# Performance work log

Hardware: AMD Instinct MI355X
Metric: run time of the kernel (lower is better)

Reference implementation:

```python
import jax, jax.numpy as jnp
import numpy as np
from jax import lax

B, S, H, T = 64, 512, 1024, 67


def setup_inputs() -> dict:
    key = jax.random.key(0)
    ks = jax.random.split(key, 8)
    hidden = jax.random.normal(ks[0], (B, S, H), jnp.float32)
    labels = jax.random.randint(ks[1], (B, S), 0, T)
    lengths = jax.random.randint(ks[2], (B,), S // 2, S + 1)
    mask = (jnp.arange(S)[None, :] < lengths[:, None]).astype(jnp.int32)  # prefix mask, mask[:,0]=1
    W = jax.random.normal(ks[3], (H, T), jnp.float32) * 0.02
    b = jnp.zeros((T,), jnp.float32)
    start_trans = jax.random.uniform(ks[4], (T,), jnp.float32, -0.1, 0.1)
    end_trans = jax.random.uniform(ks[5], (T,), jnp.float32, -0.1, 0.1)
    trans = jax.random.uniform(ks[6], (T, T), jnp.float32, -0.1, 0.1)
    return dict(hidden=hidden, labels=labels, mask=mask, W=W, b=b,
                start_trans=start_trans, end_trans=end_trans, trans=trans)


def _crf_llh(em, tags, mask, start_trans, end_trans, trans):
    # em: (B,S,T), tags: (B,S) int, mask: (B,S) bool. torchcrf log-likelihood per sequence.
    maskf = mask.astype(em.dtype)
    # numerator: score of the gold path
    em_tag = jnp.take_along_axis(em, tags[:, :, None], axis=2)[:, :, 0]       # (B,S)
    num = start_trans[tags[:, 0]] + em_tag[:, 0]
    trans_tag = trans[tags[:, :-1], tags[:, 1:]]                              # (B,S-1)
    num = num + jnp.sum((trans_tag + em_tag[:, 1:]) * maskf[:, 1:], axis=1)
    last_idx = jnp.sum(mask.astype(jnp.int32), axis=1) - 1                    # (B,)
    last_tags = jnp.take_along_axis(tags, last_idx[:, None], axis=1)[:, 0]
    num = num + end_trans[last_tags]
    # denominator: log partition via forward algorithm (scan over time)
    def step(score, x):
        em_i, m_i = x  # (B,T), (B,)
        nxt = jax.nn.logsumexp(score[:, :, None] + trans[None] + em_i[:, None, :], axis=1)
        return jnp.where(m_i[:, None], nxt, score), None
    init = start_trans[None, :] + em[:, 0]
    score, _ = lax.scan(step, init, (em[:, 1:].transpose(1, 0, 2), mask[:, 1:].T))
    denom = jax.nn.logsumexp(score + end_trans[None, :], axis=1)
    return num - denom


def _viterbi(em, mask, start_trans, end_trans, trans):
    # returns best tag sequence (B,S), padded positions set to 0
    n_tags = em.shape[-1]
    ident = jnp.arange(n_tags)[None, :]
    def fwd(score, x):
        em_i, m_i = x  # (B,T), (B,)
        cand = score[:, :, None] + trans[None]                                # (B,T,T)
        idx = jnp.argmax(cand, axis=1)                                        # (B,T)
        nxt = jnp.max(cand, axis=1) + em_i
        score = jnp.where(m_i[:, None], nxt, score)
        idx = jnp.where(m_i[:, None], idx, ident)  # identity link on padded steps
        return score, idx
    init = start_trans[None, :] + em[:, 0]
    score, hist = lax.scan(fwd, init, (em[:, 1:].transpose(1, 0, 2), mask[:, 1:].T))
    best = jnp.argmax(score + end_trans[None, :], axis=1)                     # (B,)
    def back(carry, h):  # carry = tag at t+1, h = hist[t]: (B,T)
        prev = jnp.take_along_axis(h, carry[:, None], axis=1)[:, 0]
        return prev, prev
    _, ys = lax.scan(back, best, hist, reverse=True)                          # (S-1,B) tags[0..S-2]
    tags = jnp.concatenate([ys.transpose(1, 0), best[:, None]], axis=1)       # (B,S)
    return jnp.where(mask, tags, 0)


def reference(hidden, labels, mask, W, b, start_trans, end_trans, trans):
    maskb = mask.astype(bool)
    # dropout is identity in eval mode
    em = jnp.einsum('bsh,ht->bst', jax.nn.leaky_relu(hidden, 0.01), W) + b     # token_scores
    llh = _crf_llh(em, labels, maskb, start_trans, end_trans, trans)
    loss = -jnp.sum(llh) / em.shape[0]
    tags = _viterbi(em, maskb, start_trans, end_trans, trans)
    return loss, tags, em
```

## Files before the change

kernel.cpp:

```cpp
#include <hip/hip_runtime.h>

#define Bn 64
#define Sn 512
#define Hn 1024
#define Tn 67

#define LOG2E 1.4426950408889634f
#define LN2   0.6931471805599453f

__global__ __launch_bounds__(256) void gemm_em(
    const float* __restrict__ hidden, const float* __restrict__ W,
    const float* __restrict__ bias, float* __restrict__ em,
    float* __restrict__ out)
{
    __shared__ __align__(16) float hs[64][36];
    __shared__ __align__(16) float wt[80][36];

    const int tid = threadIdx.x;
    const int tx = tid & 15, ty = tid >> 4;
    const int row0 = blockIdx.x * 64;

    if (blockIdx.x == 0 && tid == 0) out[0] = 0.0f;

    float acc[4][5];
#pragma unroll
    for (int u = 0; u < 4; ++u)
#pragma unroll
        for (int v = 0; v < 5; ++v) acc[u][v] = 0.f;

    for (int kc = 0; kc < Hn; kc += 32) {
#pragma unroll
        for (int l = 0; l < 2; ++l) {
            int idx = tid + l * 256;
            int r = idx >> 3, kq = (idx & 7) << 2;
            float4 v = *reinterpret_cast<const float4*>(
                &hidden[(size_t)(row0 + r) * Hn + kc + kq]);
            v.x = v.x > 0.f ? v.x : 0.01f * v.x;
            v.y = v.y > 0.f ? v.y : 0.01f * v.y;
            v.z = v.z > 0.f ? v.z : 0.01f * v.z;
            v.w = v.w > 0.f ? v.w : 0.01f * v.w;
            *reinterpret_cast<float4*>(&hs[r][kq]) = v;
        }
        for (int idx = tid; idx < 32 * Tn; idx += 256) {
            int k = idx / Tn;
            int t = idx - k * Tn;
            wt[t][k] = W[(size_t)(kc + k) * Tn + t];
        }
        __syncthreads();

#pragma unroll
        for (int k0 = 0; k0 < 32; k0 += 4) {
            float4 hv[4], wv[5];
#pragma unroll
            for (int u = 0; u < 4; ++u)
                hv[u] = *reinterpret_cast<float4*>(&hs[ty + 16 * u][k0]);
#pragma unroll
            for (int v = 0; v < 5; ++v)
                wv[v] = *reinterpret_cast<float4*>(&wt[tx + 16 * v][k0]);
#pragma unroll
            for (int u = 0; u < 4; ++u)
#pragma unroll
                for (int v = 0; v < 5; ++v) {
                    acc[u][v] = fmaf(hv[u].x, wv[v].x, acc[u][v]);
                    acc[u][v] = fmaf(hv[u].y, wv[v].y, acc[u][v]);
                    acc[u][v] = fmaf(hv[u].z, wv[v].z, acc[u][v]);
                    acc[u][v] = fmaf(hv[u].w, wv[v].w, acc[u][v]);
                }
        }
        __syncthreads();
    }

#pragma unroll
    for (int v = 0; v < 5; ++v) {
        int c = tx + 16 * v;
        if (c < Tn) {
            float bb = bias[c];
#pragma unroll
            for (int u = 0; u < 4; ++u) {
                int row = row0 + ty + 16 * u;
                em[(size_t)row * Tn + c] = acc[u][v] + bb;
            }
        }
    }
}

__device__ __forceinline__ unsigned long long shflx64(unsigned long long v, int m) {
    unsigned int lo = (unsigned int)v, hi = (unsigned int)(v >> 32);
    lo = __shfl_xor(lo, m);
    hi = __shfl_xor(hi, m);
    return ((unsigned long long)hi << 32) | lo;
}

__device__ __forceinline__ unsigned long long packkey(float v, int idx) {
    unsigned int b = __float_as_uint(v);
    unsigned int s = b ^ (unsigned int)(((int)b >> 31) | 0x80000000);
    return ((unsigned long long)s << 32) | (unsigned int)(127 - idx);
}

__device__ __forceinline__ float unpackval(unsigned long long key) {
    unsigned int s = (unsigned int)(key >> 32);
    unsigned int b = s ^ (unsigned int)((~(int)s >> 31) | 0x80000000);
    return __uint_as_float(b);
}

__global__ __launch_bounds__(192, 1) void crf_scan5(
    const float* __restrict__ em, const int* __restrict__ labels,
    const int* __restrict__ mask, const float* __restrict__ startT,
    const float* __restrict__ endT, const float* __restrict__ trans,
    float* __restrict__ out)
{
    __shared__ __align__(16) float emC[2][1088];
    __shared__ __align__(16) float emV[2][1088];
    __shared__ int maskC[Sn];
    __shared__ int maskV[Sn];
    __shared__ __align__(16) float pb[2][72];
    __shared__ __align__(16) float vb[2][72];
    __shared__ unsigned char hist[Sn - 1][68];
    __shared__ int tg[Sn];
    __shared__ float numSh;
    __shared__ int lenSh;

    const int tid = threadIdx.x;
    const int wid = tid >> 6;
    const int lane = tid & 63;
    const int b = blockIdx.x;
    const float* emg = em + (size_t)b * Sn * Tn;
    const int u2 = lane < 3 ? lane : 2;
    const int st2 = 64 + u2;

    if (wid == 0) {
#pragma unroll
        for (int i = 0; i < 8; ++i)
            maskC[lane + i * 64] = mask[b * Sn + lane + i * 64];

        float Ec1[68], Ec2[68];
#pragma unroll
        for (int i = 0; i < Tn; ++i) {
            Ec1[i] = exp2f(trans[i * Tn + lane] * LOG2E);
            Ec2[i] = exp2f(trans[i * Tn + st2] * LOG2E);
        }
        Ec1[67] = 0.f; Ec2[67] = 0.f;

        float sreg[17];
#pragma unroll
        for (int i = 0; i < 17; ++i) { int idx = lane + i * 64; if (idx > 1071) idx = 1071; sreg[i] = emg[idx]; }
#pragma unroll
        for (int i = 0; i < 17; ++i) {
            int idx = lane + i * 64;
            if (idx < 1072) { int s = idx / 67; emC[0][s * 68 + (idx - s * 67)] = sreg[i]; }
        }
#pragma unroll
        for (int i = 0; i < 17; ++i) { int idx = lane + i * 64; if (idx > 1071) idx = 1071; sreg[i] = emg[1072 + idx]; }

        if (lane == 0) { pb[0][67] = 0.f; pb[1][67] = 0.f; }

        float sc1 = startT[lane] + emC[0][lane];
        float sc2 = startT[st2] + emC[0][st2];
        float M = __shfl(sc1, 0);
        float p1 = exp2f((sc1 - M) * LOG2E);
        float p2 = exp2f((sc2 - M) * LOG2E);
        pb[0][lane] = p1;
        if (lane < 3) pb[0][64 + lane] = p2;
        float Mprev = M;

        for (int t = 1; t < Sn; ++t) {
            const int cb = (t >> 4) & 1;
            if ((t & 15) == 0) {
                const int k = t >> 4;
#pragma unroll
                for (int i = 0; i < 17; ++i) {
                    int idx = lane + i * 64;
                    if (idx < 1072) { int s = idx / 67; emC[cb][s * 68 + (idx - s * 67)] = sreg[i]; }
                }
                if (k < 31) {
                    const float* src = emg + (size_t)(k + 1) * 1072;
#pragma unroll
                    for (int i = 0; i < 17; ++i) { int idx = lane + i * 64; if (idx > 1071) idx = 1071; sreg[i] = src[idx]; }
                }
            }
            const float* row = &emC[cb][(t & 15) * 68];
            float em1 = row[lane];
            float em2 = row[st2];
            int m = maskC[t];
            const float4* P = (const float4*)&pb[(t + 1) & 1][0];
            float a0 = 0, a1 = 0, a2 = 0, a3 = 0, c0 = 0, c1 = 0, c2 = 0, c3 = 0;
#pragma unroll
            for (int q = 0; q < 17; ++q) {
                float4 pv = P[q];
                a0 = fmaf(pv.x, Ec1[4 * q + 0], a0); c0 = fmaf(pv.x, Ec2[4 * q + 0], c0);
                a1 = fmaf(pv.y, Ec1[4 * q + 1], a1); c1 = fmaf(pv.y, Ec2[4 * q + 1], c1);
                a2 = fmaf(pv.z, Ec1[4 * q + 2], a2); c2 = fmaf(pv.z, Ec2[4 * q + 2], c2);
                a3 = fmaf(pv.w, Ec1[4 * q + 3], a3); c3 = fmaf(pv.w, Ec2[4 * q + 3], c3);
            }
            float s1 = (a0 + a1) + (a2 + a3);
            float s2 = (c0 + c1) + (c2 + c3);
            float n1 = Mprev + log2f(s1) * LN2 + em1;
            float n2 = Mprev + log2f(s2) * LN2 + em2;
            if (m) { sc1 = n1; sc2 = n2; }
            M = __shfl(sc1, 0);
            p1 = exp2f((sc1 - M) * LOG2E);
            p2 = exp2f((sc2 - M) * LOG2E);
            float* Wp = &pb[t & 1][0];
            Wp[lane] = p1;
            if (lane < 3) Wp[64 + lane] = p2;
            Mprev = M;
        }

        float* F = &pb[0][0];
        F[lane] = sc1 + endT[lane];
        if (lane < 3) F[64 + lane] = sc2 + endT[64 + lane];
        if (lane == 0) F[67] = -1e30f;
        float mx = -1e30f;
        const float4* Fv = (const float4*)F;
#pragma unroll
        for (int q = 0; q < 17; ++q) {
            float4 v = Fv[q];
            mx = fmaxf(mx, fmaxf(fmaxf(v.x, v.y), fmaxf(v.z, v.w)));
        }
        float ss = 0.f;
#pragma unroll
        for (int q = 0; q < 17; ++q) {
            float4 v = Fv[q];
            ss += exp2f((v.x - mx) * LOG2E) + exp2f((v.y - mx) * LOG2E)
                + exp2f((v.z - mx) * LOG2E) + exp2f((v.w - mx) * LOG2E);
        }
        float denom = mx + log2f(ss) * LN2;
        __syncthreads();
        if (lane == 0) {
            int len = lenSh;
            float num = numSh + endT[labels[b * Sn + len - 1]];
            atomicAdd(out, -(num - denom) * (1.0f / (float)Bn));
        }
    } else if (wid == 1) {
#pragma unroll
        for (int i = 0; i < 8; ++i)
            maskV[lane + i * 64] = mask[b * Sn + lane + i * 64];

        float Tc1[68];
#pragma unroll
        for (int i = 0; i < Tn; ++i) Tc1[i] = trans[i * Tn + lane];
        Tc1[67] = 0.f;
        float Tsf[3], Tss[3];
        const int rsec = (lane < 3) ? (64 + lane) : 0;
#pragma unroll
        for (int u = 0; u < 3; ++u) {
            Tsf[u] = trans[lane * Tn + 64 + u];
            Tss[u] = trans[rsec * Tn + 64 + u];
        }

        float sreg[17];
#pragma unroll
        for (int i = 0; i < 17; ++i) { int idx = lane + i * 64; if (idx > 1071) idx = 1071; sreg[i] = emg[idx]; }
#pragma unroll
        for (int i = 0; i < 17; ++i) {
            int idx = lane + i * 64;
            if (idx < 1072) { int s = idx / 67; emV[0][s * 68 + (idx - s * 67)] = sreg[i]; }
        }
#pragma unroll
        for (int i = 0; i < 17; ++i) { int idx = lane + i * 64; if (idx > 1071) idx = 1071; sreg[i] = emg[1072 + idx]; }

        float sc1 = startT[lane] + emV[0][lane];
        float sc2 = startT[st2] + emV[0][st2];
        vb[0][lane] = sc1;
        if (lane < 3) vb[0][64 + lane] = sc2;
        if (lane == 0) { vb[0][67] = -1e30f; vb[1][67] = -1e30f; }

        for (int t = 1; t < Sn; ++t) {
            const int cb = (t >> 4) & 1;
            if ((t & 15) == 0) {
                const int k = t >> 4;
#pragma unroll
                for (int i = 0; i < 17; ++i) {
                    int idx = lane + i * 64;
                    if (idx < 1072) { int s = idx / 67; emV[cb][s * 68 + (idx - s * 67)] = sreg[i]; }
                }
                if (k < 31) {
                    const float* src = emg + (size_t)(k + 1) * 1072;
#pragma unroll
                    for (int i = 0; i < 17; ++i) { int idx = lane + i * 64; if (idx > 1071) idx = 1071; sreg[i] = src[idx]; }
                }
            }
            const float* row = &emV[cb][(t & 15) * 68];
            float em1 = row[lane];
            float e64 = row[64], e65 = row[65], e66 = row[66];
            int m = maskV[t];

            const float4* Vp = (const float4*)&vb[(t + 1) & 1][0];
            float bvv[34]; int bx[34];
#pragma unroll
            for (int q = 0; q < 17; ++q) {
                float4 v = Vp[q];
                float c0 = v.x + Tc1[4 * q + 0];
                float c1 = v.y + Tc1[4 * q + 1];
                float c2 = v.z + Tc1[4 * q + 2];
                float c3 = v.w + Tc1[4 * q + 3];
                bool r0 = c1 > c0;
                bvv[2 * q]     = r0 ? c1 : c0;
                bx[2 * q]      = r0 ? 4 * q + 1 : 4 * q + 0;
                bool r1 = c3 > c2;
                bvv[2 * q + 1] = r1 ? c3 : c2;
                bx[2 * q + 1]  = r1 ? 4 * q + 3 : 4 * q + 2;
            }
#pragma unroll
            for (int q = 0; q < 17; ++q) {
                bool r = bvv[2 * q + 1] > bvv[2 * q];
                bvv[q] = r ? bvv[2 * q + 1] : bvv[2 * q];
                bx[q]  = r ? bx[2 * q + 1]  : bx[2 * q];
            }
#pragma unroll
            for (int q = 0; q < 8; ++q) {
                bool r = bvv[2 * q + 1] > bvv[2 * q];
                bvv[q] = r ? bvv[2 * q + 1] : bvv[2 * q];
                bx[q]  = r ? bx[2 * q + 1]  : bx[2 * q];
            }
            bvv[8] = bvv[16]; bx[8] = bx[16];
#pragma unroll
            for (int q = 0; q < 4; ++q) {
                bool r = bvv[2 * q + 1] > bvv[2 * q];
                bvv[q] = r ? bvv[2 * q + 1] : bvv[2 * q];
                bx[q]  = r ? bx[2 * q + 1]  : bx[2 * q];
            }
            bvv[4] = bvv[8]; bx[4] = bx[8];
#pragma unroll
            for (int q = 0; q < 2; ++q) {
                bool r = bvv[2 * q + 1] > bvv[2 * q];
                bvv[q] = r ? bvv[2 * q + 1] : bvv[2 * q];
                bx[q]  = r ? bx[2 * q + 1]  : bx[2 * q];
            }
            bvv[2] = bvv[4]; bx[2] = bx[4];
            { bool r = bvv[1] > bvv[0]; bvv[0] = r ? bvv[1] : bvv[0]; bx[0] = r ? bx[1] : bx[0]; }
            { bool r = bvv[2] > bvv[0]; bvv[0] = r ? bvv[2] : bvv[0]; bx[0] = r ? bx[2] : bx[0]; }
            float n1 = bvv[0] + em1;

            float ca = sc1 + Tsf[0]; int ia = lane;
            float cbv = sc1 + Tsf[1]; int ib = lane;
            float cc = sc1 + Tsf[2]; int ic = lane;
            if (lane < 3) {
                float sa = sc2 + Tss[0]; if (sa > ca)  { ca = sa;  ia = 64 + lane; }
                float sb = sc2 + Tss[1]; if (sb > cbv) { cbv = sb; ib = 64 + lane; }
                float scv = sc2 + Tss[2]; if (scv > cc) { cc = scv; ic = 64 + lane; }
            }
            unsigned long long k0 = packkey(ca, ia);
            unsigned long long k1 = packkey(cbv, ib);
            unsigned long long k2 = packkey(cc, ic);
#pragma unroll
            for (int k = 1; k < 64; k <<= 1) {
                unsigned long long o0 = shflx64(k0, k); if (o0 > k0) k0 = o0;
                unsigned long long o1 = shflx64(k1, k); if (o1 > k1) k1 = o1;
                unsigned long long o2 = shflx64(k2, k); if (o2 > k2) k2 = o2;
            }
            float v64 = unpackval(k0) + e64;
            float v65 = unpackval(k1) + e65;
            float v66 = unpackval(k2) + e66;
            int i64 = 127 - (int)(unsigned int)(k0 & 0xffffffffu);
            int i65 = 127 - (int)(unsigned int)(k1 & 0xffffffffu);
            int i66 = 127 - (int)(unsigned int)(k2 & 0xffffffffu);

            float nuv = (lane == 0) ? v64 : (lane == 1) ? v65 : v66;
            int nui = (lane == 0) ? i64 : (lane == 1) ? i65 : i66;

            int idx1 = m ? bx[0] : lane;
            int idx2 = m ? nui : st2;
            if (m) { sc1 = n1; sc2 = nuv; }

            hist[t - 1][lane] = (unsigned char)idx1;
            float* Wv = &vb[t & 1][0];
            Wv[lane] = sc1;
            if (lane < 3) {
                hist[t - 1][64 + lane] = (unsigned char)idx2;
                Wv[64 + lane] = sc2;
            }
        }

        float* F = &vb[0][0];
        F[lane] = sc1 + endT[lane];
        if (lane < 3) F[64 + lane] = sc2 + endT[64 + lane];
        if (lane == 0) F[67] = -1e30f;
        const float4* Fv = (const float4*)F;
        float bvv[34]; int bx[34];
#pragma unroll
        for (int q = 0; q < 17; ++q) {
            float4 v = Fv[q];
            bool r0 = v.y > v.x;
            bvv[2 * q]     = r0 ? v.y : v.x;
            bx[2 * q]      = r0 ? 4 * q + 1 : 4 * q + 0;
            bool r1 = v.w > v.z;
            bvv[2 * q + 1] = r1 ? v.w : v.z;
            bx[2 * q + 1]  = r1 ? 4 * q + 3 : 4 * q + 2;
        }
#pragma unroll
        for (int q = 0; q < 17; ++q) {
            bool r = bvv[2 * q + 1] > bvv[2 * q];
            bvv[q] = r ? bvv[2 * q + 1] : bvv[2 * q];
            bx[q]  = r ? bx[2 * q + 1]  : bx[2 * q];
        }
#pragma unroll
        for (int q = 0; q < 8; ++q) {
            bool r = bvv[2 * q + 1] > bvv[2 * q];
            bvv[q] = r ? bvv[2 * q + 1] : bvv[2 * q];
            bx[q]  = r ? bx[2 * q + 1]  : bx[2 * q];
        }
        bvv[8] = bvv[16]; bx[8] = bx[16];
#pragma unroll
        for (int q = 0; q < 4; ++q) {
            bool r = bvv[2 * q + 1] > bvv[2 * q];
            bvv[q] = r ? bvv[2 * q + 1] : bvv[2 * q];
            bx[q]  = r ? bx[2 * q + 1]  : bx[2 * q];
        }
        bvv[4] = bvv[8]; bx[4] = bx[8];
#pragma unroll
        for (int q = 0; q < 2; ++q) {
            bool r = bvv[2 * q + 1] > bvv[2 * q];
            bvv[q] = r ? bvv[2 * q + 1] : bvv[2 * q];
            bx[q]  = r ? bx[2 * q + 1]  : bx[2 * q];
        }
        bvv[2] = bvv[4]; bx[2] = bx[4];
        { bool r = bvv[1] > bvv[0]; bvv[0] = r ? bvv[1] : bvv[0]; bx[0] = r ? bx[1] : bx[0]; }
        { bool r = bvv[2] > bvv[0]; bvv[0] = r ? bvv[2] : bvv[0]; bx[0] = r ? bx[2] : bx[0]; }

        if (lane == 0) {
            int carry = bx[0];
            tg[Sn - 1] = carry;
            for (int k = Sn - 2; k >= 0; --k) {
                carry = hist[k][carry];
                tg[k] = carry;
            }
        }
        float* tagsOut = out + 1 + b * Sn;
#pragma unroll
        for (int i = 0; i < 8; ++i) {
            int s = lane + i * 64;
            tagsOut[s] = maskV[s] ? (float)tg[s] : 0.f;
        }
        __syncthreads();
    } else {
        float part = 0.f; int lenp = 0;
#pragma unroll
        for (int i = 0; i < 8; ++i) {
            int s = lane + i * 64;
            int ms = mask[b * Sn + s];
            lenp += ms;
            int ls = labels[b * Sn + s];
            if (s == 0) {
                part += startT[ls] + emg[ls];
            } else if (ms) {
                int lp = labels[b * Sn + s - 1];
                part += trans[lp * Tn + ls] + emg[(size_t)s * Tn + ls];
            }
        }
#pragma unroll
        for (int k = 1; k < 64; k <<= 1) {
            part += __shfl_xor(part, k);
            lenp += __shfl_xor(lenp, k);
        }
        if (lane == 0) { numSh = part; lenSh = lenp; }
        __syncthreads();
    }
}

extern "C" void kernel_launch(void* const* d_in, const int* in_sizes, int n_in,
                              void* d_out, int out_size, void* d_ws, size_t ws_size,
                              hipStream_t stream) {
    const float* hidden = (const float*)d_in[0];
    const int*   labels = (const int*)d_in[1];
    const int*   maskp  = (const int*)d_in[2];
    const float* W      = (const float*)d_in[3];
    const float* bias   = (const float*)d_in[4];
    const float* startT = (const float*)d_in[5];
    const float* endT   = (const float*)d_in[6];
    const float* trans  = (const float*)d_in[7];
    float* out = (float*)d_out;
    float* em  = out + 1 + (size_t)Bn * Sn;

    hipLaunchKernelGGL(gemm_em, dim3((Bn * Sn) / 64), dim3(256), 0, stream,
                       hidden, W, bias, em, out);
    hipLaunchKernelGGL(crf_scan5, dim3(Bn), dim3(192), 0, stream,
                       em, labels, maskp, startT, endT, trans, out);
}
```

Baseline: 789.3 us.

## Move transition matrices from registers to LDS and reduce tail columns via shuffles

The exp-transition and raw-transition columns that each lane held in registers now live in float4-packed LDS tables read per step. The three tail tags (64-66) in the forward pass are no longer a second 68-wide dot product per lane. Each lane computes three partial products and a wavefront butterfly reduction sums them. The Viterbi argmax tree also fuses its first two levels to shorten the per-step chain. This trims register pressure and redundant FMAs, but adds LDS reads and a six-stage shuffle chain to every serial scan step.

```diff
diff --git a/kernel.cpp b/kernel.cpp
--- a/kernel.cpp
+++ b/kernel.cpp
@@ -103,7 +103,7 @@
     return __uint_as_float(b);
 }
 
-__global__ __launch_bounds__(192, 1) void crf_scan5(
+__global__ __launch_bounds__(192, 1) void crf_scan6(
     const float* __restrict__ em, const int* __restrict__ labels,
     const int* __restrict__ mask, const float* __restrict__ startT,
     const float* __restrict__ endT, const float* __restrict__ trans,
@@ -115,6 +115,8 @@
     __shared__ int maskV[Sn];
     __shared__ __align__(16) float pb[2][72];
     __shared__ __align__(16) float vb[2][72];
+    __shared__ __align__(16) float4 EcT[17 * 68];
+    __shared__ __align__(16) float4 TcT[17 * 68];
     __shared__ unsigned char hist[Sn - 1][68];
     __shared__ int tg[Sn];
     __shared__ float numSh;
@@ -133,13 +135,22 @@
         for (int i = 0; i < 8; ++i)
             maskC[lane + i * 64] = mask[b * Sn + lane + i * 64];
 
-        float Ec1[68], Ec2[68];
-#pragma unroll
-        for (int i = 0; i < Tn; ++i) {
-            Ec1[i] = exp2f(trans[i * Tn + lane] * LOG2E);
-            Ec2[i] = exp2f(trans[i * Tn + st2] * LOG2E);
-        }
-        Ec1[67] = 0.f; Ec2[67] = 0.f;
+        for (int idx = lane; idx < 17 * 68; idx += 64) {
+            int i4 = idx / 68, j = idx - i4 * 68;
+            float4 e;
+            int i0 = 4 * i4;
+            e.x = (i0 + 0 < Tn && j < Tn) ? exp2f(trans[(i0 + 0) * Tn + j] * LOG2E) : 0.f;
+            e.y = (i0 + 1 < Tn && j < Tn) ? exp2f(trans[(i0 + 1) * Tn + j] * LOG2E) : 0.f;
+            e.z = (i0 + 2 < Tn && j < Tn) ? exp2f(trans[(i0 + 2) * Tn + j] * LOG2E) : 0.f;
+            e.w = (i0 + 3 < Tn && j < Tn) ? exp2f(trans[(i0 + 3) * Tn + j] * LOG2E) : 0.f;
+            EcT[idx] = e;
+        }
+        float Esf[3], Ess[3];
+#pragma unroll
+        for (int u = 0; u < 3; ++u) {
+            Esf[u] = exp2f(trans[lane * Tn + 64 + u] * LOG2E);
+            Ess[u] = exp2f(trans[st2 * Tn + 64 + u] * LOG2E);
+        }
 
         float sreg[17];
 #pragma unroll
@@ -182,18 +193,34 @@
             float em1 = row[lane];
             float em2 = row[st2];
             int m = maskC[t];
+
             const float4* P = (const float4*)&pb[(t + 1) & 1][0];
-            float a0 = 0, a1 = 0, a2 = 0, a3 = 0, c0 = 0, c1 = 0, c2 = 0, c3 = 0;
+            float a0 = 0, a1 = 0, a2 = 0, a3 = 0;
 #pragma unroll
             for (int q = 0; q < 17; ++q) {
                 float4 pv = P[q];
-                a0 = fmaf(pv.x, Ec1[4 * q + 0], a0); c0 = fmaf(pv.x, Ec2[4 * q + 0], c0);
-                a1 = fmaf(pv.y, Ec1[4 * q + 1], a1); c1 = fmaf(pv.y, Ec2[4 * q + 1], c1);
-                a2 = fmaf(pv.z, Ec1[4 * q + 2], a2); c2 = fmaf(pv.z, Ec2[4 * q + 2], c2);
-                a3 = fmaf(pv.w, Ec1[4 * q + 3], a3); c3 = fmaf(pv.w, Ec2[4 * q + 3], c3);
+                float4 e = EcT[q * 68 + lane];
+                a0 = fmaf(pv.x, e.x, a0);
+                a1 = fmaf(pv.y, e.y, a1);
+                a2 = fmaf(pv.z, e.z, a2);
+                a3 = fmaf(pv.w, e.w, a3);
             }
             float s1 = (a0 + a1) + (a2 + a3);
-            float s2 = (c0 + c1) + (c2 + c3);
+
+            float g0 = p1 * Esf[0], g1 = p1 * Esf[1], g2 = p1 * Esf[2];
+            if (lane < 3) {
+                g0 = fmaf(p2, Ess[0], g0);
+                g1 = fmaf(p2, Ess[1], g1);
+                g2 = fmaf(p2, Ess[2], g2);
+            }
+#pragma unroll
+            for (int k = 1; k < 64; k <<= 1) {
+                g0 += __shfl_xor(g0, k);
+                g1 += __shfl_xor(g1, k);
+                g2 += __shfl_xor(g2, k);
+            }
+            float s2 = (u2 == 0) ? g0 : (u2 == 1) ? g1 : g2;
+
             float n1 = Mprev + log2f(s1) * LN2 + em1;
             float n2 = Mprev + log2f(s2) * LN2 + em2;
             if (m) { sc1 = n1; sc2 = n2; }
@@ -236,10 +263,16 @@
         for (int i = 0; i < 8; ++i)
             maskV[lane + i * 64] = mask[b * Sn + lane + i * 64];
 
-        float Tc1[68];
-#pragma unroll
-        for (int i = 0; i < Tn; ++i) Tc1[i] = trans[i * Tn + lane];
-        Tc1[67] = 0.f;
+        for (int idx = lane; idx < 17 * 68; idx += 64) {
+            int i4 = idx / 68, j = idx - i4 * 68;
+            float4 e;
+            int i0 = 4 * i4;
+            e.x = (i0 + 0 < Tn && j < Tn) ? trans[(i0 + 0) * Tn + j] : 0.f;
+            e.y = (i0 + 1 < Tn && j < Tn) ? trans[(i0 + 1) * Tn + j] : 0.f;
+            e.z = (i0 + 2 < Tn && j < Tn) ? trans[(i0 + 2) * Tn + j] : 0.f;
+            e.w = (i0 + 3 < Tn && j < Tn) ? trans[(i0 + 3) * Tn + j] : 0.f;
+            TcT[idx] = e;
+        }
         float Tsf[3], Tss[3];
         const int rsec = (lane < 3) ? (64 + lane) : 0;
 #pragma unroll
@@ -286,51 +319,46 @@
             int m = maskV[t];
 
             const float4* Vp = (const float4*)&vb[(t + 1) & 1][0];
-            float bvv[34]; int bx[34];
+            float bv[17]; int bi[17];
 #pragma unroll
             for (int q = 0; q < 17; ++q) {
                 float4 v = Vp[q];
-                float c0 = v.x + Tc1[4 * q + 0];
-                float c1 = v.y + Tc1[4 * q + 1];
-                float c2 = v.z + Tc1[4 * q + 2];
-                float c3 = v.w + Tc1[4 * q + 3];
+                float4 tt = TcT[q * 68 + lane];
+                float c0 = v.x + tt.x;
+                float c1 = v.y + tt.y;
+                float c2 = v.z + tt.z;
+                float c3 = v.w + tt.w;
                 bool r0 = c1 > c0;
-                bvv[2 * q]     = r0 ? c1 : c0;
-                bx[2 * q]      = r0 ? 4 * q + 1 : 4 * q + 0;
+                float m01v = r0 ? c1 : c0; int m01i = r0 ? 4 * q + 1 : 4 * q + 0;
                 bool r1 = c3 > c2;
-                bvv[2 * q + 1] = r1 ? c3 : c2;
-                bx[2 * q + 1]  = r1 ? 4 * q + 3 : 4 * q + 2;
-            }
-#pragma unroll
-            for (int q = 0; q < 17; ++q) {
-                bool r = bvv[2 * q + 1] > bvv[2 * q];
-                bvv[q] = r ? bvv[2 * q + 1] : bvv[2 * q];
-                bx[q]  = r ? bx[2 * q + 1]  : bx[2 * q];
+                float m23v = r1 ? c3 : c2; int m23i = r1 ? 4 * q + 3 : 4 * q + 2;
+                bool r2 = m23v > m01v;
+                bv[q] = r2 ? m23v : m01v; bi[q] = r2 ? m23i : m01i;
             }
 #pragma unroll
             for (int q = 0; q < 8; ++q) {
-                bool r = bvv[2 * q + 1] > bvv[2 * q];
-                bvv[q] = r ? bvv[2 * q + 1] : bvv[2 * q];
-                bx[q]  = r ? bx[2 * q + 1]  : bx[2 * q];
-            }
-            bvv[8] = bvv[16]; bx[8] = bx[16];
+                bool r = bv[2 * q + 1] > bv[2 * q];
+                bv[q] = r ? bv[2 * q + 1] : bv[2 * q];
+                bi[q] = r ? bi[2 * q + 1] : bi[2 * q];
+            }
+            bv[8] = bv[16]; bi[8] = bi[16];
 #pragma unroll
             for (int q = 0; q < 4; ++q) {
-                bool r = bvv[2 * q + 1] > bvv[2 * q];
-                bvv[q] = r ? bvv[2 * q + 1] : bvv[2 * q];
-                bx[q]  = r ? bx[2 * q + 1]  : bx[2 * q];
-            }
-            bvv[4] = bvv[8]; bx[4] = bx[8];
+                bool r = bv[2 * q + 1] > bv[2 * q];
+                bv[q] = r ? bv[2 * q + 1] : bv[2 * q];
+                bi[q] = r ? bi[2 * q + 1] : bi[2 * q];
+            }
+            bv[4] = bv[8]; bi[4] = bi[8];
 #pragma unroll
             for (int q = 0; q < 2; ++q) {
-                bool r = bvv[2 * q + 1] > bvv[2 * q];
-                bvv[q] = r ? bvv[2 * q + 1] : bvv[2 * q];
-                bx[q]  = r ? bx[2 * q + 1]  : bx[2 * q];
-            }
-            bvv[2] = bvv[4]; bx[2] = bx[4];
-            { bool r = bvv[1] > bvv[0]; bvv[0] = r ? bvv[1] : bvv[0]; bx[0] = r ? bx[1] : bx[0]; }
-            { bool r = bvv[2] > bvv[0]; bvv[0] = r ? bvv[2] : bvv[0]; bx[0] = r ? bx[2] : bx[0]; }
-            float n1 = bvv[0] + em1;
+                bool r = bv[2 * q + 1] > bv[2 * q];
+                bv[q] = r ? bv[2 * q + 1] : bv[2 * q];
+                bi[q] = r ? bi[2 * q + 1] : bi[2 * q];
+            }
+            bv[2] = bv[4]; bi[2] = bi[4];
+            { bool r = bv[1] > bv[0]; bv[0] = r ? bv[1] : bv[0]; bi[0] = r ? bi[1] : bi[0]; }
+            { bool r = bv[2] > bv[0]; bv[0] = r ? bv[2] : bv[0]; bi[0] = r ? bi[2] : bi[0]; }
+            float n1 = bv[0] + em1;
 
             float ca = sc1 + Tsf[0]; int ia = lane;
             float cbv = sc1 + Tsf[1]; int ib = lane;
@@ -359,7 +387,7 @@
             float nuv = (lane == 0) ? v64 : (lane == 1) ? v65 : v66;
             int nui = (lane == 0) ? i64 : (lane == 1) ? i65 : i66;
 
-            int idx1 = m ? bx[0] : lane;
+            int idx1 = m ? bi[0] : lane;
             int idx2 = m ? nui : st2;
             if (m) { sc1 = n1; sc2 = nuv; }
 
@@ -377,49 +405,43 @@
         if (lane < 3) F[64 + lane] = sc2 + endT[64 + lane];
         if (lane == 0) F[67] = -1e30f;
         const float4* Fv = (const float4*)F;
-        float bvv[34]; int bx[34];
+        float bv[17]; int bi[17];
 #pragma unroll
         for (int q = 0; q < 17; ++q) {
             float4 v = Fv[q];
             bool r0 = v.y > v.x;
-            bvv[2 * q]     = r0 ? v.y : v.x;
-            bx[2 * q]      = r0 ? 4 * q + 1 : 4 * q + 0;
+            float m01v = r0 ? v.y : v.x; int m01i = r0 ? 4 * q + 1 : 4 * q + 0;
             bool r1 = v.w > v.z;
-            bvv[2 * q + 1] = r1 ? v.w : v.z;
-            bx[2 * q + 1]  = r1 ? 4 * q + 3 : 4 * q + 2;
-        }
-#pragma unroll
-        for (int q = 0; q < 17; ++q) {
-            bool r = bvv[2 * q + 1] > bvv[2 * q];
-            bvv[q] = r ? bvv[2 * q + 1] : bvv[2 * q];
-            bx[q]  = r ? bx[2 * q + 1]  : bx[2 * q];
+            float m23v = r1 ? v.w : v.z; int m23i = r1 ? 4 * q + 3 : 4 * q + 2;
+            bool r2 = m23v > m01v;
+            bv[q] = r2 ? m23v : m01v; bi[q] = r2 ? m23i : m01i;
         }
 #pragma unroll
         for (int q = 0; q < 8; ++q) {
-            bool r = bvv[2 * q + 1] > bvv[2 * q];
-            bvv[q] = r ? bvv[2 * q + 1] : bvv[2 * q];
-            bx[q]  = r ? bx[2 * q + 1]  : bx[2 * q];
-        }
-        bvv[8] = bvv[16]; bx[8] = bx[16];
+            bool r = bv[2 * q + 1] > bv[2 * q];
+            bv[q] = r ? bv[2 * q + 1] : bv[2 * q];
+            bi[q] = r ? bi[2 * q + 1] : bi[2 * q];
+        }
+        bv[8] = bv[16]; bi[8] = bi[16];
 #pragma unroll
         for (int q = 0; q < 4; ++q) {
-            bool r = bvv[2 * q + 1] > bvv[2 * q];
-            bvv[q] = r ? bvv[2 * q + 1] : bvv[2 * q];
-            bx[q]  = r ? bx[2 * q + 1]  : bx[2 * q];
-        }
-        bvv[4] = bvv[8]; bx[4] = bx[8];
+            bool r = bv[2 * q + 1] > bv[2 * q];
+            bv[q] = r ? bv[2 * q + 1] : bv[2 * q];
+            bi[q] = r ? bi[2 * q + 1] : bi[2 * q];
+        }
+        bv[4] = bv[8]; bi[4] = bi[8];
 #pragma unroll
         for (int q = 0; q < 2; ++q) {
-            bool r = bvv[2 * q + 1] > bvv[2 * q];
-            bvv[q] = r ? bvv[2 * q + 1] : bvv[2 * q];
-            bx[q]  = r ? bx[2 * q + 1]  : bx[2 * q];
-        }
-        bvv[2] = bvv[4]; bx[2] = bx[4];
-        { bool r = bvv[1] > bvv[0]; bvv[0] = r ? bvv[1] : bvv[0]; bx[0] = r ? bx[1] : bx[0]; }
-        { bool r = bvv[2] > bvv[0]; bvv[0] = r ? bvv[2] : bvv[0]; bx[0] = r ? bx[2] : bx[0]; }
+            bool r = bv[2 * q + 1] > bv[2 * q];
+            bv[q] = r ? bv[2 * q + 1] : bv[2 * q];
+            bi[q] = r ? bi[2 * q + 1] : bi[2 * q];
+        }
+        bv[2] = bv[4]; bi[2] = bi[4];
+        { bool r = bv[1] > bv[0]; bv[0] = r ? bv[1] : bv[0]; bi[0] = r ? bi[1] : bi[0]; }
+        { bool r = bv[2] > bv[0]; bv[0] = r ? bv[2] : bv[0]; bi[0] = r ? bi[2] : bi[0]; }
 
         if (lane == 0) {
-            int carry = bx[0];
+            int carry = bi[0];
             tg[Sn - 1] = carry;
             for (int k = Sn - 2; k >= 0; --k) {
                 carry = hist[k][carry];
@@ -474,6 +496,6 @@
 
     hipLaunchKernelGGL(gemm_em, dim3((Bn * Sn) / 64), dim3(256), 0, stream,
                        hidden, W, bias, em, out);
-    hipLaunchKernelGGL(crf_scan5, dim3(Bn), dim3(192), 0, stream,
+    hipLaunchKernelGGL(crf_scan6, dim3(Bn), dim3(192), 0, stream,
                        em, labels, maskp, startT, endT, trans, out);
 }
```

New measurement: 1.394 ms. 1.77x slower.
